# Optimization experiments

Measured on AMD Instinct MI355X. Metric: run time of the kernel, lower is better.

## Reference

```python
import jax, jax.numpy as jnp
import numpy as np

IN_DIMS = 4
DEPTH = 4
C = IN_DIMS + 1                     # channels after time augmentation
SIG = sum(C ** k for k in range(1, DEPTH + 1))  # 780
N, T = 64, 1024


def setup_inputs() -> dict:
    key = jax.random.key(0)
    k1, k2, k3, k4, k5 = jax.random.split(key, 5)
    batch = jax.random.normal(k1, (N, T, IN_DIMS), dtype=jnp.float32)
    s_c = 1.0 / np.sqrt(C)
    conv_w = jax.random.normal(k2, (C, C), dtype=jnp.float32) * s_c
    conv_b = jax.random.normal(k3, (C,), dtype=jnp.float32) * s_c
    s_l = 1.0 / np.sqrt(SIG)
    lin_w = jax.random.normal(k4, (SIG, SIG), dtype=jnp.float32) * s_l
    lin_b = jax.random.normal(k5, (SIG,), dtype=jnp.float32) * s_l
    return {"batch": batch, "conv_w": conv_w, "conv_b": conv_b,
            "lin_w": lin_w, "lin_b": lin_b}


def _stream_signature(path):
    """Streamed path signature with zero basepoint.

    path: (n, t, C). Returns (n, t, SIG) where entry t is the signature of
    the piecewise-linear path (0, path[0], ..., path[t]) truncated at DEPTH,
    levels flattened in lexicographic (row-major) order like signatory.
    """
    n = path.shape[0]
    # increments; basepoint=True means first increment is path[:,0] - 0
    dx = jnp.concatenate([path[:, :1, :], path[:, 1:, :] - path[:, :-1, :]], axis=1)
    init = tuple(jnp.zeros((n, C ** k), path.dtype) for k in range(1, DEPTH + 1))

    def step(levels, d):
        # exp(d) in the truncated tensor algebra: e_k = d^{(x)k} / k!
        e = [d]
        for k in range(2, DEPTH + 1):
            e.append((jnp.einsum('na,nb->nab', e[-1], d) / k).reshape(n, -1))
        # Chen: new_k = e_k + S_k + sum_{i=1}^{k-1} S_i (x) e_{k-i}
        new = []
        for k in range(1, DEPTH + 1):
            acc = levels[k - 1] + e[k - 1]
            for i in range(1, k):
                acc = acc + jnp.einsum('na,nb->nab', levels[i - 1], e[k - i - 1]).reshape(n, -1)
            new.append(acc)
        new = tuple(new)
        return new, jnp.concatenate(new, axis=-1)

    _, ys = jax.lax.scan(step, init, jnp.swapaxes(dx, 0, 1))  # ys: (t, n, SIG)
    return jnp.swapaxes(ys, 0, 1)


def reference(batch, conv_w, conv_b, lin_w, lin_b):
    n, t, _ = batch.shape
    # time augmentation: append channel arange(1,T+1)/T
    time = (jnp.arange(1, t + 1, dtype=batch.dtype) / t)[None, :, None]
    a = jnp.concatenate([batch, jnp.broadcast_to(time, (n, t, 1))], axis=-1)  # (n,t,C)
    # kernel-size-1 conv1d == pointwise linear over channels
    b = a @ conv_w.T + conv_b                                                  # (n,t,C)
    c = _stream_signature(b)                                                   # (n,t,SIG)
    # zero out the first stream entry (torch.concat of zeros with c[:,1:,:])
    c = jnp.concatenate([jnp.zeros((n, 1, SIG), c.dtype), c[:, 1:, :]], axis=1)
    return jnp.tanh(c @ lin_w.T + lin_b)
```

## Files before the change

kernel.cpp:

```cpp
#include <hip/hip_runtime.h>
#include <math.h>

#define N_B 64
#define T_LEN 1024
#define IN_D 4
#define CH 5
#define SIG 780
#define KP 800
#define SEG_LEN 16
#define N_SEG 64
#define SC_L1 1.0f
#define SC_L2 0.25f
#define SC_L3 0.0625f
#define SC_L4 0.015625f

typedef _Float16 f16x8 __attribute__((ext_vector_type(8)));
typedef float f32x4 __attribute__((ext_vector_type(4)));

typedef __attribute__((address_space(1))) const void* as1cp;
typedef __attribute__((address_space(3))) void* as3p;

__device__ __forceinline__ float fast_tanh(float x) {
  float ax = fabsf(x);
  float e = __expf(-2.0f * ax);
  float r = (1.0f - e) * __builtin_amdgcn_rcpf(1.0f + e);
  return copysignf(r, x);
}

__global__ __launch_bounds__(256) void conv_kernel(
    const float* __restrict__ batch,
    const float* __restrict__ conv_w,
    const float* __restrict__ conv_b,
    float* __restrict__ b_out) {
  int idx = blockIdx.x * blockDim.x + threadIdx.x;
  if (idx >= N_B * T_LEN) return;
  int t = idx & (T_LEN - 1);
  const float* a = batch + (size_t)idx * IN_D;
  float a0 = a[0], a1 = a[1], a2 = a[2], a3 = a[3];
  float tm = (float)(t + 1) / (float)T_LEN;
  float* o = b_out + (size_t)idx * CH;
#pragma unroll
  for (int j = 0; j < CH; ++j) {
    const float* w = conv_w + j * CH;
    float r = conv_b[j];
    r = fmaf(tm, w[4], r);
    r = fmaf(a3, w[3], r);
    r = fmaf(a2, w[2], r);
    r = fmaf(a1, w[1], r);
    r = fmaf(a0, w[0], r);
    o[j] = r;
  }
}

__global__ __launch_bounds__(320) void seg_kernel(
    const float* __restrict__ batch,
    const float* __restrict__ conv_w,
    const float* __restrict__ conv_b,
    float* __restrict__ P) {
  int s = blockIdx.x;
  int n = blockIdx.y;
  int tid = threadIdx.x;

  __shared__ float S[SIG];
  __shared__ float bc[(SEG_LEN + 1) * CH];
  __shared__ float dsh[SEG_LEN][CH];

  for (int i = tid; i < SIG; i += 320) S[i] = 0.0f;
  if (tid < (SEG_LEN + 1) * CH) {
    int r = s * SEG_LEN - 1 + tid / CH, ch = tid % CH;
    float v = 0.0f;
    if (r >= 0) {
      const float* a = batch + ((size_t)n * T_LEN + r) * IN_D;
      const float* w = conv_w + ch * CH;
      v = conv_b[ch];
      v = fmaf(a[0], w[0], v);
      v = fmaf(a[1], w[1], v);
      v = fmaf(a[2], w[2], v);
      v = fmaf(a[3], w[3], v);
      v = fmaf((float)(r + 1) * (1.0f / T_LEN), w[4], v);
    }
    bc[tid] = v;
  }
  __syncthreads();
  if (tid < SEG_LEN * CH) {
    int j = tid / CH, ch = tid % CH;
    dsh[j][ch] = bc[(j + 1) * CH + ch] - bc[j * CH + ch];
  }

  const int x0 = tid;
  const int x1 = tid + 320;
  const bool has1 = (tid < 305);
  const int a0i = x0 / 125, b0i = (x0 / 25) % 5, c0i = (x0 / 5) % 5, d0i = x0 % 5;
  const int a1i = x1 / 125, b1i = (x1 / 25) % 5, c1i = (x1 / 5) % 5, d1i = x1 % 5;
  const int s2_0 = x0 / 25, s3_0 = x0 / 5;
  const int s2_1 = x1 / 25, s3_1 = x1 / 5;
  const bool hasL3 = (tid < 125);
  const int ya = tid / 25, yb = (tid / 5) % 5, yc = tid % 5;
  const bool hasL2 = (tid < 25);
  const int za = tid / 5, zb = tid % 5;
  const bool hasL1 = (tid < CH);
  __syncthreads();

  for (int j = 0; j < SEG_LEN; ++j) {
    float n4_0, n4_1 = 0.0f, n3 = 0.0f, n2 = 0.0f, n1 = 0.0f;
    {
      float tH = fmaf(0.25f, dsh[j][a0i], S[a0i]);
      tH = fmaf((1.0f / 3.0f) * dsh[j][b0i], tH, S[5 + s2_0]);
      tH = fmaf(0.5f * dsh[j][c0i], tH, S[30 + s3_0]);
      n4_0 = fmaf(dsh[j][d0i], tH, S[155 + x0]);
    }
    if (has1) {
      float tH = fmaf(0.25f, dsh[j][a1i], S[a1i]);
      tH = fmaf((1.0f / 3.0f) * dsh[j][b1i], tH, S[5 + s2_1]);
      tH = fmaf(0.5f * dsh[j][c1i], tH, S[30 + s3_1]);
      n4_1 = fmaf(dsh[j][d1i], tH, S[155 + x1]);
    }
    if (hasL3) {
      float tH = fmaf((1.0f / 3.0f), dsh[j][ya], S[ya]);
      tH = fmaf(0.5f * dsh[j][yb], tH, S[5 + ya * 5 + yb]);
      n3 = fmaf(dsh[j][yc], tH, S[30 + tid]);
    }
    if (hasL2) {
      float tH = fmaf(0.5f, dsh[j][za], S[za]);
      n2 = fmaf(dsh[j][zb], tH, S[5 + tid]);
    }
    if (hasL1) n1 = S[tid] + dsh[j][tid];
    __syncthreads();
    S[155 + x0] = n4_0;
    if (has1) S[155 + x1] = n4_1;
    if (hasL3) S[30 + tid] = n3;
    if (hasL2) S[5 + tid] = n2;
    if (hasL1) S[tid] = n1;
    __syncthreads();
  }

  float* Pr = P + ((size_t)n * N_SEG + s) * SIG;
  for (int i = tid; i < SIG; i += 320) Pr[i] = S[i];
}

__global__ __launch_bounds__(640) void prefix_kernel(float* __restrict__ P) {
  int n = blockIdx.x;
  int tid = threadIdx.x;
  __shared__ float A[SIG];
  __shared__ float Bs[SIG];

  float* Pn = P + (size_t)n * N_SEG * SIG;
  for (int i = tid; i < SIG; i += 640) A[i] = Pn[i];
  int i0 = tid, i1 = tid + 640;
  float r0 = 0.f, r1 = 0.f;
  if (i0 < SIG) r0 = Pn[SIG + i0];
  if (i1 < SIG) r1 = Pn[SIG + i1];

  const int e4 = tid;
  const int q4a = e4 / 125, r125 = e4 % 125, r25 = e4 % 25, r5 = e4 % 5;
  const int e4d5 = e4 / 5, e4d25 = e4 / 25;
  const int e3 = tid;
  const int e3a = e3 / 25, e3r25 = e3 % 25, e3r5 = e3 % 5, e3d5 = e3 / 5;
  const int e2 = tid - 125;
  const int e1 = tid - 150;

  for (int s = 1; s < N_SEG; ++s) {
    if (i0 < SIG) Bs[i0] = r0;
    if (i1 < SIG) Bs[i1] = r1;
    __syncthreads();
    if (s + 1 < N_SEG) {
      const float* Pnx = Pn + (size_t)(s + 1) * SIG;
      if (i0 < SIG) r0 = Pnx[i0];
      if (i1 < SIG) r1 = Pnx[i1];
    }
    float v4 = 0.f, v3 = 0.f, v2 = 0.f, v1 = 0.f;
    if (tid < 625) {
      v4 = A[155 + e4] + Bs[155 + e4];
      v4 = fmaf(A[30 + e4d5], Bs[r5], v4);
      v4 = fmaf(A[5 + e4d25], Bs[5 + r25], v4);
      v4 = fmaf(A[q4a], Bs[30 + r125], v4);
    }
    if (tid < 125) {
      v3 = A[30 + e3] + Bs[30 + e3];
      v3 = fmaf(A[5 + e3d5], Bs[e3r5], v3);
      v3 = fmaf(A[e3a], Bs[5 + e3r25], v3);
    } else if (tid < 150) {
      v2 = A[5 + e2] + Bs[5 + e2];
      v2 = fmaf(A[e2 / 5], Bs[e2 % 5], v2);
    } else if (tid < 155) {
      v1 = A[e1] + Bs[e1];
    }
    __syncthreads();
    float* Po = Pn + (size_t)s * SIG;
    if (tid < 625) { A[155 + e4] = v4; Po[155 + e4] = v4; }
    if (tid < 125) { A[30 + e3] = v3; Po[30 + e3] = v3; }
    else if (tid < 150) { A[5 + e2] = v2; Po[5 + e2] = v2; }
    else if (tid < 155) { A[e1] = v1; Po[e1] = v1; }
  }
}

__global__ __launch_bounds__(320) void emit_kernel(
    const float* __restrict__ batch,
    const float* __restrict__ conv_w,
    const float* __restrict__ conv_b,
    const float* __restrict__ P,
    _Float16* __restrict__ c1,
    _Float16* __restrict__ c2) {
  int s = blockIdx.x;
  int n = blockIdx.y;
  int tid = threadIdx.x;

  __shared__ float S[SIG];
  __shared__ float bc[(SEG_LEN + 1) * CH];
  __shared__ float dsh[SEG_LEN][CH];
  __shared__ __align__(16) _Float16 row1[KP];
  __shared__ __align__(16) _Float16 row2[KP];

  if (s == 0) {
    for (int i = tid; i < SIG; i += 320) S[i] = 0.0f;
  } else {
    const float* Pr = P + ((size_t)n * N_SEG + (s - 1)) * SIG;
    for (int i = tid; i < SIG; i += 320) S[i] = Pr[i];
  }
  if (tid < (SEG_LEN + 1) * CH) {
    int r = s * SEG_LEN - 1 + tid / CH, ch = tid % CH;
    float v = 0.0f;
    if (r >= 0) {
      const float* a = batch + ((size_t)n * T_LEN + r) * IN_D;
      const float* w = conv_w + ch * CH;
      v = conv_b[ch];
      v = fmaf(a[0], w[0], v);
      v = fmaf(a[1], w[1], v);
      v = fmaf(a[2], w[2], v);
      v = fmaf(a[3], w[3], v);
      v = fmaf((float)(r + 1) * (1.0f / T_LEN), w[4], v);
    }
    bc[tid] = v;
  }
  if (tid < KP - SIG) {
    row1[SIG + tid] = (_Float16)0.0f;
    row2[SIG + tid] = (_Float16)0.0f;
  }
  __syncthreads();
  if (tid < SEG_LEN * CH) {
    int j = tid / CH, ch = tid % CH;
    dsh[j][ch] = bc[(j + 1) * CH + ch] - bc[j * CH + ch];
  }

  const int x0 = tid;
  const int x1 = tid + 320;
  const bool has1 = (tid < 305);
  const int a0i = x0 / 125, b0i = (x0 / 25) % 5, c0i = (x0 / 5) % 5, d0i = x0 % 5;
  const int a1i = x1 / 125, b1i = (x1 / 25) % 5, c1i = (x1 / 5) % 5, d1i = x1 % 5;
  const int s2_0 = x0 / 25, s3_0 = x0 / 5;
  const int s2_1 = x1 / 25, s3_1 = x1 / 5;
  const bool hasL3 = (tid < 125);
  const int ya = tid / 25, yb = (tid / 5) % 5, yc = tid % 5;
  const bool hasL2 = (tid < 25);
  const int za = tid / 5, zb = tid % 5;
  const bool hasL1 = (tid < CH);
  __syncthreads();

  for (int j = 0; j < SEG_LEN; ++j) {
    int t = s * SEG_LEN + j;
    float n4_0, n4_1 = 0.0f, n3 = 0.0f, n2 = 0.0f, n1 = 0.0f;
    {
      float tH = fmaf(0.25f, dsh[j][a0i], S[a0i]);
      tH = fmaf((1.0f / 3.0f) * dsh[j][b0i], tH, S[5 + s2_0]);
      tH = fmaf(0.5f * dsh[j][c0i], tH, S[30 + s3_0]);
      n4_0 = fmaf(dsh[j][d0i], tH, S[155 + x0]);
    }
    if (has1) {
      float tH = fmaf(0.25f, dsh[j][a1i], S[a1i]);
      tH = fmaf((1.0f / 3.0f) * dsh[j][b1i], tH, S[5 + s2_1]);
      tH = fmaf(0.5f * dsh[j][c1i], tH, S[30 + s3_1]);
      n4_1 = fmaf(dsh[j][d1i], tH, S[155 + x1]);
    }
    if (hasL3) {
      float tH = fmaf((1.0f / 3.0f), dsh[j][ya], S[ya]);
      tH = fmaf(0.5f * dsh[j][yb], tH, S[5 + ya * 5 + yb]);
      n3 = fmaf(dsh[j][yc], tH, S[30 + tid]);
    }
    if (hasL2) {
      float tH = fmaf(0.5f, dsh[j][za], S[za]);
      n2 = fmaf(dsh[j][zb], tH, S[5 + tid]);
    }
    if (hasL1) n1 = S[tid] + dsh[j][tid];
    __syncthreads();

    S[155 + x0] = n4_0;
    if (has1) S[155 + x1] = n4_1;
    if (hasL3) S[30 + tid] = n3;
    if (hasL2) S[5 + tid] = n2;
    if (hasL1) S[tid] = n1;

    float z = (t == 0) ? 0.0f : 1.0f;
    {
      float v = n4_0 * SC_L4 * z;
      _Float16 h = (_Float16)v;
      row1[155 + x0] = h; row2[155 + x0] = (_Float16)(v - (float)h);
    }
    if (has1) {
      float v = n4_1 * SC_L4 * z;
      _Float16 h = (_Float16)v;
      row1[155 + x1] = h; row2[155 + x1] = (_Float16)(v - (float)h);
    }
    if (hasL3) {
      float v = n3 * SC_L3 * z;
      _Float16 h = (_Float16)v;
      row1[30 + tid] = h; row2[30 + tid] = (_Float16)(v - (float)h);
    }
    if (hasL2) {
      float v = n2 * SC_L2 * z;
      _Float16 h = (_Float16)v;
      row1[5 + tid] = h; row2[5 + tid] = (_Float16)(v - (float)h);
    }
    if (hasL1) {
      float v = n1 * SC_L1 * z;
      _Float16 h = (_Float16)v;
      row1[tid] = h; row2[tid] = (_Float16)(v - (float)h);
    }
    __syncthreads();

    size_t base = ((size_t)n * T_LEN + t) * KP;
    if (tid < 100) {
      *(float4*)(c1 + base + tid * 8) = *(const float4*)&row1[tid * 8];
    } else if (tid < 200) {
      int c = tid - 100;
      *(float4*)(c2 + base + c * 8) = *(const float4*)&row2[c * 8];
    }
  }
}

__global__ __launch_bounds__(256) void wconv_kernel(
    const float* __restrict__ W,
    _Float16* __restrict__ w1,
    _Float16* __restrict__ w2) {
  int idx = blockIdx.x * blockDim.x + threadIdx.x;
  if (idx >= 896 * KP) return;
  int nn = idx / KP, k = idx % KP;
  float v = 0.0f;
  if (nn < SIG && k < SIG) {
    float sc = (k < 5) ? 1.0f : (k < 30) ? 4.0f : (k < 155) ? 16.0f : 64.0f;
    v = W[(size_t)nn * SIG + k] * sc;
  }
  _Float16 h = (_Float16)v;
  w1[idx] = h;
  w2[idx] = (_Float16)(v - (float)h);
}

__global__ __launch_bounds__(256) void gemm_mfma(
    const _Float16* __restrict__ A1p, const _Float16* __restrict__ A2p,
    const _Float16* __restrict__ B1p, const _Float16* __restrict__ B2p,
    const float* __restrict__ bias, float* __restrict__ out) {
  __shared__ _Float16 Al[2][2][128 * 32];
  __shared__ _Float16 Bl[2][2][128 * 32];

  int tid = threadIdx.x;
  int lane = tid & 63, wid = tid >> 6;
  int wm = wid >> 1, wn = wid & 1;
  int m0 = blockIdx.y * 128;
  int n0 = blockIdx.x * 128;

  f32x4 acc[4][4];
#pragma unroll
  for (int i = 0; i < 4; ++i)
#pragma unroll
    for (int j = 0; j < 4; ++j) acc[i][j] = (f32x4){0.f, 0.f, 0.f, 0.f};

  int sr = lane >> 2, scn = lane & 3;
  int swst = (sr ^ (sr >> 2)) & 3;
  int qg = scn ^ swst;
  int fr = lane & 15, fq = lane >> 4;
  int swf = (fr ^ (fr >> 2)) & 3;
  int fchunk = fq ^ swf;

  auto stage = [&](int kb, int buf) {
    int k0 = kb * 32;
#pragma unroll
    for (int i = 0; i < 2; ++i) {
      int rloc = wid * 16 + i * 64 + sr;
      size_t gA = (size_t)(m0 + rloc) * KP + k0 + qg * 8;
      size_t gB = (size_t)(n0 + rloc) * KP + k0 + qg * 8;
      int lb = (wid * 16 + i * 64) * 32;
      __builtin_amdgcn_global_load_lds((as1cp)(A1p + gA), (as3p)(&Al[buf][0][lb]), 16, 0, 0);
      __builtin_amdgcn_global_load_lds((as1cp)(A2p + gA), (as3p)(&Al[buf][1][lb]), 16, 0, 0);
      __builtin_amdgcn_global_load_lds((as1cp)(B1p + gB), (as3p)(&Bl[buf][0][lb]), 16, 0, 0);
      __builtin_amdgcn_global_load_lds((as1cp)(B2p + gB), (as3p)(&Bl[buf][1][lb]), 16, 0, 0);
    }
  };

  stage(0, 0);
  for (int kb = 0; kb < 25; ++kb) {
    int cur = kb & 1;
    __syncthreads();
    f16x8 a1[4], a2[4], b1[4], b2[4];
#pragma unroll
    for (int tm = 0; tm < 4; ++tm) {
      int off = (wm * 64 + tm * 16 + fr) * 32 + fchunk * 8;
      a1[tm] = *(const f16x8*)&Al[cur][0][off];
      a2[tm] = *(const f16x8*)&Al[cur][1][off];
    }
#pragma unroll
    for (int tn = 0; tn < 4; ++tn) {
      int off = (wn * 64 + tn * 16 + fr) * 32 + fchunk * 8;
      b1[tn] = *(const f16x8*)&Bl[cur][0][off];
      b2[tn] = *(const f16x8*)&Bl[cur][1][off];
    }
    if (kb < 24) stage(kb + 1, cur ^ 1);
#pragma unroll
    for (int tm = 0; tm < 4; ++tm)
#pragma unroll
      for (int tn = 0; tn < 4; ++tn) {
        acc[tm][tn] = __builtin_amdgcn_mfma_f32_16x16x32_f16(a1[tm], b1[tn], acc[tm][tn], 0, 0, 0);
        acc[tm][tn] = __builtin_amdgcn_mfma_f32_16x16x32_f16(a1[tm], b2[tn], acc[tm][tn], 0, 0, 0);
        acc[tm][tn] = __builtin_amdgcn_mfma_f32_16x16x32_f16(a2[tm], b1[tn], acc[tm][tn], 0, 0, 0);
      }
  }
  __syncthreads();

  float* ep = (float*)((wid < 2) ? (void*)&Al[0][0][0] : (void*)&Bl[0][0][0]);
  ep += (wid & 1) * 4096;

  float bv[4];
#pragma unroll
  for (int tn = 0; tn < 4; ++tn) {
    int nn = n0 + wn * 64 + tn * 16 + fr;
    bv[tn] = (nn < SIG) ? bias[nn] : 0.0f;
  }
#pragma unroll
  for (int h = 0; h < 2; ++h) {
#pragma unroll
    for (int tm2 = 0; tm2 < 2; ++tm2) {
      int tm = h * 2 + tm2;
#pragma unroll
      for (int tn = 0; tn < 4; ++tn) {
#pragma unroll
        for (int r = 0; r < 4; ++r) {
          int lr = tm2 * 16 + fq * 4 + r;
          int lc = tn * 16 + fr;
          ep[lr * 66 + lc] = fast_tanh(acc[tm][tn][r] + bv[tn]);
        }
      }
    }
#pragma unroll
    for (int p = 0; p < 2; ++p) {
      int lr = lane & 31;
      int ck = (lane >> 5) * 2 + p;
      int gm = m0 + wm * 64 + h * 32 + lr;
      int gc0 = n0 + wn * 64 + ck * 16;
#pragma unroll
      for (int q = 0; q < 4; ++q) {
        int col = gc0 + q * 4;
        if (col + 3 < SIG) {
          *(float4*)(out + (size_t)gm * SIG + col) =
              *(const float4*)&ep[lr * 66 + ck * 16 + q * 4];
        } else if (col < SIG) {
#pragma unroll
          for (int e = 0; e < 4; ++e) {
            int c2 = col + e;
            if (c2 < SIG) out[(size_t)gm * SIG + c2] = ep[lr * 66 + ck * 16 + q * 4 + e];
          }
        }
      }
    }
  }
}

__global__ __launch_bounds__(320) void sig_kernel_fb(
    const float* __restrict__ b_in, float* __restrict__ c_out) {
  int n = blockIdx.x;
  int tid = threadIdx.x;
  __shared__ float S[SIG];
  __shared__ float bc[64 * CH];
  __shared__ float dsh[CH];
  __shared__ float pb[CH];
  for (int i = tid; i < SIG; i += 320) S[i] = 0.0f;
  if (tid < CH) pb[tid] = 0.0f;
  const float* bn = b_in + (size_t)n * T_LEN * CH;
  float* cn = c_out + (size_t)n * T_LEN * SIG;
// ... 125 lines not shown
    }
  }
}

extern "C" void kernel_launch(void* const* d_in, const int* in_sizes, int n_in,
                              void* d_out, int out_size, void* d_ws, size_t ws_size,
                              hipStream_t stream) {
  const float* batch = (const float*)d_in[0];
  const float* conv_w = (const float*)d_in[1];
  const float* conv_b = (const float*)d_in[2];
  const float* lin_w = (const float*)d_in[3];
  const float* lin_b = (const float*)d_in[4];
  float* out = (float*)d_out;

  const size_t plane_elems = (size_t)N_B * T_LEN * KP;
  const size_t wplane_elems = (size_t)896 * KP;
  const size_t P_elems = (size_t)N_B * N_SEG * SIG;
  const size_t bp_elems = (size_t)N_B * T_LEN * CH;
  const size_t need_big = 2 * plane_elems * sizeof(_Float16) +
                          2 * wplane_elems * sizeof(_Float16) +
                          P_elems * sizeof(float);

  if (ws_size >= need_big) {
    _Float16* c1 = (_Float16*)d_ws;
    _Float16* c2 = c1 + plane_elems;
    _Float16* w1 = c2 + plane_elems;
    _Float16* w2 = w1 + wplane_elems;
    float* P = (float*)(w2 + wplane_elems);

    wconv_kernel<<<dim3((896 * KP + 255) / 256), dim3(256), 0, stream>>>(
        lin_w, w1, w2);
    seg_kernel<<<dim3(N_SEG, N_B), dim3(320), 0, stream>>>(batch, conv_w, conv_b, P);
    prefix_kernel<<<dim3(N_B), dim3(640), 0, stream>>>(P);
    emit_kernel<<<dim3(N_SEG, N_B), dim3(320), 0, stream>>>(
        batch, conv_w, conv_b, P, c1, c2);
    gemm_mfma<<<dim3(7, 512), dim3(256), 0, stream>>>(c1, c2, w1, w2, lin_b, out);
  } else {
    float* b_path = (float*)d_ws;
    float* c_sig = (float*)d_ws + bp_elems;
    conv_kernel<<<dim3((N_B * T_LEN + 255) / 256), dim3(256), 0, stream>>>(
        batch, conv_w, conv_b, b_path);
    sig_kernel_fb<<<dim3(N_B), dim3(320), 0, stream>>>(b_path, c_sig);
    gemm_tanh_fb<<<dim3((N_B * T_LEN) / BM, (SIG + BN - 1) / BN), dim3(256), 0, stream>>>(
        c_sig, lin_w, lin_b, out);
  }
}
```

Baseline: 724.5 us.

## Use single-wave segment kernels with register-held level 4 and loop GEMM over N tiles

```diff
diff --git a/kernel.cpp b/kernel.cpp
--- a/kernel.cpp
+++ b/kernel.cpp
@@ -7,6 +7,7 @@
 #define CH 5
 #define SIG 780
 #define KP 800
+#define NPAD 896
 #define SEG_LEN 16
 #define N_SEG 64
 #define SC_L1 1.0f
@@ -25,6 +26,507 @@
   float e = __expf(-2.0f * ax);
   float r = (1.0f - e) * __builtin_amdgcn_rcpf(1.0f + e);
   return copysignf(r, x);
+}
+
+__device__ __forceinline__ float sel5(float d0, float d1, float d2, float d3,
+                                      float d4, int i) {
+  float r = d0;
+  r = (i == 1) ? d1 : r;
+  r = (i == 2) ? d2 : r;
+  r = (i == 3) ? d3 : r;
+  r = (i == 4) ? d4 : r;
+  return r;
+}
+
+
+__global__ __launch_bounds__(64) void seg_wave(
+    const float* __restrict__ batch,
+    const float* __restrict__ conv_w,
+    const float* __restrict__ conv_b,
+    float* __restrict__ P) {
+  int s = blockIdx.x;
+  int n = blockIdx.y;
+  int lane = threadIdx.x;
+
+  __shared__ float S123[160];
+  __shared__ float bc[85];
+  __shared__ float dsh[SEG_LEN][CH];
+
+  for (int i = lane; i < 160; i += 64) S123[i] = 0.0f;
+#pragma unroll
+  for (int p = 0; p < 2; ++p) {
+    int e = lane + p * 64;
+    if (e < (SEG_LEN + 1) * CH) {
+      int r = s * SEG_LEN - 1 + e / CH, ch = e % CH;
+      float v = 0.0f;
+      if (r >= 0) {
+        const float* a = batch + ((size_t)n * T_LEN + r) * IN_D;
+        const float* w = conv_w + ch * CH;
+        v = conv_b[ch];
+        v = fmaf(a[0], w[0], v);
+        v = fmaf(a[1], w[1], v);
+        v = fmaf(a[2], w[2], v);
+        v = fmaf(a[3], w[3], v);
+        v = fmaf((float)(r + 1) * (1.0f / T_LEN), w[4], v);
+      }
+      bc[e] = v;
+    }
+  }
+  __syncthreads();
+#pragma unroll
+  for (int p = 0; p < 2; ++p) {
+    int e = lane + p * 64;
+    if (e < SEG_LEN * CH) dsh[e / CH][e % CH] = bc[e + CH] - bc[e];
+  }
+  __syncthreads();
+
+  const int xb = lane * 10;
+  const int a_lo = xb / 125, a_hi = (xb + 9) / 125;
+  const int s2_lo = xb / 25, s2_hi = (xb + 9) / 25;
+  const int s3_lo = 2 * lane, s3_hi = 2 * lane + 1;
+  const int b_lo = s2_lo % 5, b_hi = s2_hi % 5;
+  const int c_lo = s3_lo % 5, c_hi = s3_hi % 5;
+  const int q_a = a_lo * 125 + 125 - xb;
+  const int q_b = s2_lo * 25 + 25 - xb;
+  const int y0 = lane, y1 = lane + 64;
+  const bool hy0 = (y0 < 125), hy1 = (y1 < 125);
+  const int y0a = y0 / 25, y0s = y0 / 5, y0b = y0s % 5, y0c = y0 % 5;
+  const int y1a = y1 / 25, y1s = y1 / 5, y1b = y1s % 5, y1c = y1 % 5;
+  const bool hz = (lane < 25);
+  const int za = lane / 5, zb = lane % 5;
+  const bool h1 = (lane < 5);
+
+  float S4r[10];
+#pragma unroll
+  for (int q = 0; q < 10; ++q) S4r[q] = 0.0f;
+
+  for (int j = 0; j < SEG_LEN; ++j) {
+    float dr0 = dsh[j][0], dr1 = dsh[j][1], dr2 = dsh[j][2], dr3 = dsh[j][3],
+          dr4 = dsh[j][4];
+    float drA[5] = {dr0, dr1, dr2, dr3, dr4};
+    float da_l = sel5(dr0, dr1, dr2, dr3, dr4, a_lo);
+    float da_h = sel5(dr0, dr1, dr2, dr3, dr4, a_hi);
+    float db_l = sel5(dr0, dr1, dr2, dr3, dr4, b_lo);
+    float db_h = sel5(dr0, dr1, dr2, dr3, dr4, b_hi);
+    float dc_l = sel5(dr0, dr1, dr2, dr3, dr4, c_lo);
+    float dc_h = sel5(dr0, dr1, dr2, dr3, dr4, c_hi);
+    float s1_l = S123[a_lo], s1_h = S123[a_hi];
+    float s2v_l = S123[5 + s2_lo], s2v_h = S123[5 + s2_hi];
+    float s3v_l = S123[30 + s3_lo], s3v_h = S123[30 + s3_hi];
+
+#pragma unroll
+    for (int q = 0; q < 10; ++q) {
+      bool ua = (q >= q_a), ub = (q >= q_b);
+      float s1 = ua ? s1_h : s1_l, da = ua ? da_h : da_l;
+      float s2v = ub ? s2v_h : s2v_l, db = ub ? db_h : db_l;
+      float s3v = (q < 5) ? s3v_l : s3v_h;
+      float dc = (q < 5) ? dc_l : dc_h;
+      float dd = drA[q % 5];
+      float tH = fmaf(0.25f, da, s1);
+      tH = fmaf((1.0f / 3.0f) * db, tH, s2v);
+      tH = fmaf(0.5f * dc, tH, s3v);
+      S4r[q] = fmaf(dd, tH, S4r[q]);
+    }
+
+    float n3_0 = 0.f, n3_1 = 0.f, n2 = 0.f, n1 = 0.f;
+    if (hy0) {
+      float tH = fmaf((1.0f / 3.0f), drA[0] * 0.f + dsh[j][y0a], S123[y0a]);
+      tH = fmaf(0.5f * dsh[j][y0b], tH, S123[5 + y0s]);
+      n3_0 = fmaf(dsh[j][y0c], tH, S123[30 + y0]);
+    }
+    if (hy1) {
+      float tH = fmaf((1.0f / 3.0f), dsh[j][y1a], S123[y1a]);
+      tH = fmaf(0.5f * dsh[j][y1b], tH, S123[5 + y1s]);
+      n3_1 = fmaf(dsh[j][y1c], tH, S123[30 + y1]);
+    }
+    if (hz) {
+      float tH = fmaf(0.5f, dsh[j][za], S123[za]);
+      n2 = fmaf(dsh[j][zb], tH, S123[5 + lane]);
+    }
+    if (h1) n1 = S123[lane] + dsh[j][lane];
+    __syncthreads();
+    if (hy0) S123[30 + y0] = n3_0;
+    if (hy1) S123[30 + y1] = n3_1;
+    if (hz) S123[5 + lane] = n2;
+    if (h1) S123[lane] = n1;
+    __syncthreads();
+  }
+
+  float* Pr = P + ((size_t)n * N_SEG + s) * SIG;
+  for (int i = lane; i < 155; i += 64) Pr[i] = S123[i];
+#pragma unroll
+  for (int q = 0; q < 10; ++q) {
+    int x = xb + q;
+    if (x < 625) Pr[155 + x] = S4r[q];
+  }
+}
+
+__global__ __launch_bounds__(640) void prefix_kernel(float* __restrict__ P) {
+  int n = blockIdx.x;
+  int tid = threadIdx.x;
+  __shared__ float A[SIG];
+  __shared__ float Bs[SIG];
+
+  float* Pn = P + (size_t)n * N_SEG * SIG;
+  for (int i = tid; i < SIG; i += 640) A[i] = Pn[i];
+  int i0 = tid, i1 = tid + 640;
+  float r0 = 0.f, r1 = 0.f;
+  if (i0 < SIG) r0 = Pn[SIG + i0];
+  if (i1 < SIG) r1 = Pn[SIG + i1];
+
+  const int e4 = tid;
+  const int q4a = e4 / 125, r125 = e4 % 125, r25 = e4 % 25, r5 = e4 % 5;
+  const int e4d5 = e4 / 5, e4d25 = e4 / 25;
+  const int e3 = tid;
+  const int e3a = e3 / 25, e3r25 = e3 % 25, e3r5 = e3 % 5, e3d5 = e3 / 5;
+  const int e2 = tid - 125;
+  const int e1 = tid - 150;
+
+  for (int s = 1; s < N_SEG; ++s) {
+    if (i0 < SIG) Bs[i0] = r0;
+    if (i1 < SIG) Bs[i1] = r1;
+    __syncthreads();
+    if (s + 1 < N_SEG) {
+      const float* Pnx = Pn + (size_t)(s + 1) * SIG;
+      if (i0 < SIG) r0 = Pnx[i0];
+      if (i1 < SIG) r1 = Pnx[i1];
+    }
+    float v4 = 0.f, v3 = 0.f, v2 = 0.f, v1 = 0.f;
+    if (tid < 625) {
+      v4 = A[155 + e4] + Bs[155 + e4];
+      v4 = fmaf(A[30 + e4d5], Bs[r5], v4);
+      v4 = fmaf(A[5 + e4d25], Bs[5 + r25], v4);
+      v4 = fmaf(A[q4a], Bs[30 + r125], v4);
+    }
+    if (tid < 125) {
+      v3 = A[30 + e3] + Bs[30 + e3];
+      v3 = fmaf(A[5 + e3d5], Bs[e3r5], v3);
+      v3 = fmaf(A[e3a], Bs[5 + e3r25], v3);
+    } else if (tid < 150) {
+      v2 = A[5 + e2] + Bs[5 + e2];
+      v2 = fmaf(A[e2 / 5], Bs[e2 % 5], v2);
+    } else if (tid < 155) {
+      v1 = A[e1] + Bs[e1];
+    }
+    __syncthreads();
+    float* Po = Pn + (size_t)s * SIG;
+    if (tid < 625) { A[155 + e4] = v4; Po[155 + e4] = v4; }
+    if (tid < 125) { A[30 + e3] = v3; Po[30 + e3] = v3; }
+    else if (tid < 150) { A[5 + e2] = v2; Po[5 + e2] = v2; }
+    else if (tid < 155) { A[e1] = v1; Po[e1] = v1; }
+  }
+}
+
+__global__ __launch_bounds__(64) void emit_wave(
+    const float* __restrict__ batch,
+    const float* __restrict__ conv_w,
+    const float* __restrict__ conv_b,
+    const float* __restrict__ P,
+    _Float16* __restrict__ c1,
+    _Float16* __restrict__ c2) {
+  int s = blockIdx.x;
+  int n = blockIdx.y;
+  int lane = threadIdx.x;
+
+  __shared__ float S123[160];
+  __shared__ float bc[85];
+  __shared__ float dsh[SEG_LEN][CH];
+  __shared__ __align__(16) _Float16 row1[KP];
+  __shared__ __align__(16) _Float16 row2[KP];
+
+  const int xb = lane * 10;
+  float S4r[10];
+  if (s == 0) {
+    for (int i = lane; i < 160; i += 64) S123[i] = 0.0f;
+#pragma unroll
+    for (int q = 0; q < 10; ++q) S4r[q] = 0.0f;
+  } else {
+    const float* Pr = P + ((size_t)n * N_SEG + (s - 1)) * SIG;
+    for (int i = lane; i < 155; i += 64) S123[i] = Pr[i];
+    if (lane < 5) S123[155 + lane] = 0.0f;
+#pragma unroll
+    for (int q = 0; q < 10; ++q) {
+      int x = xb + q;
+      S4r[q] = (x < 625) ? Pr[155 + x] : 0.0f;
+    }
+  }
+#pragma unroll
+  for (int p = 0; p < 2; ++p) {
+    int e = lane + p * 64;
+    if (e < (SEG_LEN + 1) * CH) {
+      int r = s * SEG_LEN - 1 + e / CH, ch = e % CH;
+      float v = 0.0f;
+      if (r >= 0) {
+        const float* a = batch + ((size_t)n * T_LEN + r) * IN_D;
+        const float* w = conv_w + ch * CH;
+        v = conv_b[ch];
+        v = fmaf(a[0], w[0], v);
+        v = fmaf(a[1], w[1], v);
+        v = fmaf(a[2], w[2], v);
+        v = fmaf(a[3], w[3], v);
+        v = fmaf((float)(r + 1) * (1.0f / T_LEN), w[4], v);
+      }
+      bc[e] = v;
+    }
+  }
+  if (lane < KP - SIG) {
+    row1[SIG + lane] = (_Float16)0.0f;
+    row2[SIG + lane] = (_Float16)0.0f;
+  }
+  __syncthreads();
+#pragma unroll
+  for (int p = 0; p < 2; ++p) {
+    int e = lane + p * 64;
+    if (e < SEG_LEN * CH) dsh[e / CH][e % CH] = bc[e + CH] - bc[e];
+  }
+  __syncthreads();
+
+  const int a_lo = xb / 125, a_hi = (xb + 9) / 125;
+  const int s2_lo = xb / 25, s2_hi = (xb + 9) / 25;
+  const int s3_lo = 2 * lane, s3_hi = 2 * lane + 1;
+  const int b_lo = s2_lo % 5, b_hi = s2_hi % 5;
+  const int c_lo = s3_lo % 5, c_hi = s3_hi % 5;
+  const int q_a = a_lo * 125 + 125 - xb;
+  const int q_b = s2_lo * 25 + 25 - xb;
+  const int y0 = lane, y1 = lane + 64;
+  const bool hy0 = (y0 < 125), hy1 = (y1 < 125);
+  const int y0a = y0 / 25, y0s = y0 / 5, y0b = y0s % 5, y0c = y0 % 5;
+  const int y1a = y1 / 25, y1s = y1 / 5, y1b = y1s % 5, y1c = y1 % 5;
+  const bool hz = (lane < 25);
+  const int za = lane / 5, zb = lane % 5;
+  const bool h1 = (lane < 5);
+
+  for (int j = 0; j < SEG_LEN; ++j) {
+    int t = s * SEG_LEN + j;
+    float zf = (t == 0) ? 0.0f : 1.0f;
+    float dr0 = dsh[j][0], dr1 = dsh[j][1], dr2 = dsh[j][2], dr3 = dsh[j][3],
+          dr4 = dsh[j][4];
+    float drA[5] = {dr0, dr1, dr2, dr3, dr4};
+    float da_l = sel5(dr0, dr1, dr2, dr3, dr4, a_lo);
+    float da_h = sel5(dr0, dr1, dr2, dr3, dr4, a_hi);
+    float db_l = sel5(dr0, dr1, dr2, dr3, dr4, b_lo);
+    float db_h = sel5(dr0, dr1, dr2, dr3, dr4, b_hi);
+    float dc_l = sel5(dr0, dr1, dr2, dr3, dr4, c_lo);
+    float dc_h = sel5(dr0, dr1, dr2, dr3, dr4, c_hi);
+    float s1_l = S123[a_lo], s1_h = S123[a_hi];
+    float s2v_l = S123[5 + s2_lo], s2v_h = S123[5 + s2_hi];
+    float s3v_l = S123[30 + s3_lo], s3v_h = S123[30 + s3_hi];
+
+#pragma unroll
+    for (int q = 0; q < 10; ++q) {
+      bool ua = (q >= q_a), ub = (q >= q_b);
+      float s1 = ua ? s1_h : s1_l, da = ua ? da_h : da_l;
+      float s2v = ub ? s2v_h : s2v_l, db = ub ? db_h : db_l;
+      float s3v = (q < 5) ? s3v_l : s3v_h;
+      float dc = (q < 5) ? dc_l : dc_h;
+      float dd = drA[q % 5];
+      float tH = fmaf(0.25f, da, s1);
+      tH = fmaf((1.0f / 3.0f) * db, tH, s2v);
+      tH = fmaf(0.5f * dc, tH, s3v);
+      S4r[q] = fmaf(dd, tH, S4r[q]);
+    }
+
+    float n3_0 = 0.f, n3_1 = 0.f, n2 = 0.f, n1 = 0.f;
+    if (hy0) {
+      float tH = fmaf((1.0f / 3.0f), dsh[j][y0a], S123[y0a]);
+      tH = fmaf(0.5f * dsh[j][y0b], tH, S123[5 + y0s]);
+      n3_0 = fmaf(dsh[j][y0c], tH, S123[30 + y0]);
+    }
+    if (hy1) {
+      float tH = fmaf((1.0f / 3.0f), dsh[j][y1a], S123[y1a]);
+      tH = fmaf(0.5f * dsh[j][y1b], tH, S123[5 + y1s]);
+      n3_1 = fmaf(dsh[j][y1c], tH, S123[30 + y1]);
+    }
+    if (hz) {
+      float tH = fmaf(0.5f, dsh[j][za], S123[za]);
+      n2 = fmaf(dsh[j][zb], tH, S123[5 + lane]);
+    }
+    if (h1) n1 = S123[lane] + dsh[j][lane];
+    __syncthreads();
+
+    if (hy0) S123[30 + y0] = n3_0;
+    if (hy1) S123[30 + y1] = n3_1;
+    if (hz) S123[5 + lane] = n2;
+    if (h1) S123[lane] = n1;
+#pragma unroll
+    for (int q = 0; q < 10; ++q) {
+      int x = xb + q;
+      if (x < 625) {
+        float v = S4r[q] * (SC_L4 * zf);
+        _Float16 h = (_Float16)v;
+        row1[155 + x] = h;
+        row2[155 + x] = (_Float16)(v - (float)h);
+      }
+    }
+    if (hy0) {
+      float v = n3_0 * (SC_L3 * zf);
+      _Float16 h = (_Float16)v;
+      row1[30 + y0] = h; row2[30 + y0] = (_Float16)(v - (float)h);
+    }
+    if (hy1) {
+      float v = n3_1 * (SC_L3 * zf);
+      _Float16 h = (_Float16)v;
+      row1[30 + y1] = h; row2[30 + y1] = (_Float16)(v - (float)h);
+    }
+    if (hz) {
+      float v = n2 * (SC_L2 * zf);
+      _Float16 h = (_Float16)v;
+      row1[5 + lane] = h; row2[5 + lane] = (_Float16)(v - (float)h);
+    }
+    if (h1) {
+      float v = n1 * (SC_L1 * zf);
+      _Float16 h = (_Float16)v;
+      row1[lane] = h; row2[lane] = (_Float16)(v - (float)h);
+    }
+    __syncthreads();
+
+    size_t base = ((size_t)n * T_LEN + t) * KP;
+    *(float4*)(c1 + base + lane * 8) = *(const float4*)&row1[lane * 8];
+    *(float4*)(c2 + base + lane * 8) = *(const float4*)&row2[lane * 8];
+    if (lane < 36) {
+      *(float4*)(c1 + base + (64 + lane) * 8) = *(const float4*)&row1[(64 + lane) * 8];
+      *(float4*)(c2 + base + (64 + lane) * 8) = *(const float4*)&row2[(64 + lane) * 8];
+    }
+  }
+}
+
+__global__ __launch_bounds__(256) void wconv_kernel(
+    const float* __restrict__ W,
+    _Float16* __restrict__ w1,
+    _Float16* __restrict__ w2) {
+  int idx = blockIdx.x * blockDim.x + threadIdx.x;
+  if (idx >= NPAD * KP) return;
+  int nn = idx / KP, k = idx % KP;
+  float v = 0.0f;
+  if (nn < SIG && k < SIG) {
+    float sc = (k < 5) ? 1.0f : (k < 30) ? 4.0f : (k < 155) ? 16.0f : 64.0f;
+    v = W[(size_t)nn * SIG + k] * sc;
+  }
+  _Float16 h = (_Float16)v;
+  w1[idx] = h;
+  w2[idx] = (_Float16)(v - (float)h);
+}
+
+__global__ __launch_bounds__(256) void gemm_mfma(
+    const _Float16* __restrict__ A1p, const _Float16* __restrict__ A2p,
+    const _Float16* __restrict__ B1p, const _Float16* __restrict__ B2p,
+    const float* __restrict__ bias, float* __restrict__ out) {
+  __shared__ _Float16 Al[2][2][128 * 32];
+  __shared__ _Float16 Bl[2][2][128 * 32];
+
+  int tid = threadIdx.x;
+  int lane = tid & 63, wid = tid >> 6;
+  int wm = wid >> 1, wn = wid & 1;
+  int m0 = blockIdx.x * 128;
+
+  int sr = lane >> 2, scn = lane & 3;
+  int swst = (sr ^ (sr >> 2)) & 3;
+  int qg = scn ^ swst;
+  int fr = lane & 15, fq = lane >> 4;
+  int swf = (fr ^ (fr >> 2)) & 3;
+  int fchunk = fq ^ swf;
+
+  auto stage = [&](int n0, int kb, int buf) {
+    int k0 = kb * 32;
+#pragma unroll
+    for (int i = 0; i < 2; ++i) {
+      int rloc = wid * 16 + i * 64 + sr;
+      size_t gA = (size_t)(m0 + rloc) * KP + k0 + qg * 8;
+      size_t gB = (size_t)(n0 + rloc) * KP + k0 + qg * 8;
+      int lb = (wid * 16 + i * 64) * 32;
+      __builtin_amdgcn_global_load_lds((as1cp)(A1p + gA), (as3p)(&Al[buf][0][lb]), 16, 0, 0);
+      __builtin_amdgcn_global_load_lds((as1cp)(A2p + gA), (as3p)(&Al[buf][1][lb]), 16, 0, 0);
+      __builtin_amdgcn_global_load_lds((as1cp)(B1p + gB), (as3p)(&Bl[buf][0][lb]), 16, 0, 0);
+      __builtin_amdgcn_global_load_lds((as1cp)(B2p + gB), (as3p)(&Bl[buf][1][lb]), 16, 0, 0);
+    }
+  };
+
+  for (int nt = 0; nt < 7; ++nt) {
+    int n0 = nt * 128;
+
+    f32x4 acc[4][4];
+#pragma unroll
+    for (int i = 0; i < 4; ++i)
+#pragma unroll
+      for (int j = 0; j < 4; ++j) acc[i][j] = (f32x4){0.f, 0.f, 0.f, 0.f};
+
+    stage(n0, 0, 0);
+    for (int kb = 0; kb < 25; ++kb) {
+      int cur = kb & 1;
+      __syncthreads();
+      f16x8 a1[4], a2[4], b1[4], b2[4];
+#pragma unroll
+      for (int tm = 0; tm < 4; ++tm) {
+        int off = (wm * 64 + tm * 16 + fr) * 32 + fchunk * 8;
+        a1[tm] = *(const f16x8*)&Al[cur][0][off];
+        a2[tm] = *(const f16x8*)&Al[cur][1][off];
+      }
+#pragma unroll
+      for (int tn = 0; tn < 4; ++tn) {
+        int off = (wn * 64 + tn * 16 + fr) * 32 + fchunk * 8;
+        b1[tn] = *(const f16x8*)&Bl[cur][0][off];
+        b2[tn] = *(const f16x8*)&Bl[cur][1][off];
+      }
+      if (kb < 24) stage(n0, kb + 1, cur ^ 1);
+#pragma unroll
+      for (int tm = 0; tm < 4; ++tm)
+#pragma unroll
+        for (int tn = 0; tn < 4; ++tn) {
+          acc[tm][tn] = __builtin_amdgcn_mfma_f32_16x16x32_f16(a1[tm], b1[tn], acc[tm][tn], 0, 0, 0);
+          acc[tm][tn] = __builtin_amdgcn_mfma_f32_16x16x32_f16(a1[tm], b2[tn], acc[tm][tn], 0, 0, 0);
+          acc[tm][tn] = __builtin_amdgcn_mfma_f32_16x16x32_f16(a2[tm], b1[tn], acc[tm][tn], 0, 0, 0);
+        }
+    }
+    __syncthreads();
+
+    float* ep = (float*)((wid < 2) ? (void*)&Al[0][0][0] : (void*)&Bl[0][0][0]);
+    ep += (wid & 1) * 4096;
+
+    float bv[4];
+#pragma unroll
+    for (int tn = 0; tn < 4; ++tn) {
+      int nn = n0 + wn * 64 + tn * 16 + fr;
+      bv[tn] = (nn < SIG) ? bias[nn] : 0.0f;
+    }
+#pragma unroll
+    for (int h = 0; h < 2; ++h) {
+#pragma unroll
+      for (int tm2 = 0; tm2 < 2; ++tm2) {
+        int tm = h * 2 + tm2;
+#pragma unroll
+        for (int tn = 0; tn < 4; ++tn) {
+#pragma unroll
+          for (int r = 0; r < 4; ++r) {
+            int lr = tm2 * 16 + fq * 4 + r;
+            int lc = tn * 16 + fr;
+            ep[lr * 66 + lc] = fast_tanh(acc[tm][tn][r] + bv[tn]);
+          }
+        }
+      }
+#pragma unroll
+      for (int p = 0; p < 2; ++p) {
+        int lr = lane & 31;
+        int ck = (lane >> 5) * 2 + p;
+        int gm = m0 + wm * 64 + h * 32 + lr;
+        int gc0 = n0 + wn * 64 + ck * 16;
+#pragma unroll
+        for (int q = 0; q < 4; ++q) {
+          int col = gc0 + q * 4;
+          if (col + 3 < SIG) {
+            *(float4*)(out + (size_t)gm * SIG + col) =
+                *(const float4*)&ep[lr * 66 + ck * 16 + q * 4];
+          } else if (col < SIG) {
+#pragma unroll
+            for (int e = 0; e < 4; ++e) {
+              int c2 = col + e;
+              if (c2 < SIG) out[(size_t)gm * SIG + c2] = ep[lr * 66 + ck * 16 + q * 4 + e];
+            }
+          }
+        }
+      }
+    }
+    __syncthreads();
+  }
 }
 
 __global__ __launch_bounds__(256) void conv_kernel(
@@ -49,416 +551,6 @@
     r = fmaf(a1, w[1], r);
     r = fmaf(a0, w[0], r);
     o[j] = r;
-  }
-}
-
-__global__ __launch_bounds__(320) void seg_kernel(
-    const float* __restrict__ batch,
-    const float* __restrict__ conv_w,
-    const float* __restrict__ conv_b,
-    float* __restrict__ P) {
-  int s = blockIdx.x;
-  int n = blockIdx.y;
-  int tid = threadIdx.x;
-
-  __shared__ float S[SIG];
-  __shared__ float bc[(SEG_LEN + 1) * CH];
-  __shared__ float dsh[SEG_LEN][CH];
-
-  for (int i = tid; i < SIG; i += 320) S[i] = 0.0f;
-  if (tid < (SEG_LEN + 1) * CH) {
-    int r = s * SEG_LEN - 1 + tid / CH, ch = tid % CH;
-    float v = 0.0f;
-    if (r >= 0) {
-      const float* a = batch + ((size_t)n * T_LEN + r) * IN_D;
-      const float* w = conv_w + ch * CH;
-      v = conv_b[ch];
-      v = fmaf(a[0], w[0], v);
-      v = fmaf(a[1], w[1], v);
-      v = fmaf(a[2], w[2], v);
-      v = fmaf(a[3], w[3], v);
-      v = fmaf((float)(r + 1) * (1.0f / T_LEN), w[4], v);
-    }
-    bc[tid] = v;
-  }
-  __syncthreads();
-  if (tid < SEG_LEN * CH) {
-    int j = tid / CH, ch = tid % CH;
-    dsh[j][ch] = bc[(j + 1) * CH + ch] - bc[j * CH + ch];
-  }
-
-  const int x0 = tid;
-  const int x1 = tid + 320;
-  const bool has1 = (tid < 305);
-  const int a0i = x0 / 125, b0i = (x0 / 25) % 5, c0i = (x0 / 5) % 5, d0i = x0 % 5;
-  const int a1i = x1 / 125, b1i = (x1 / 25) % 5, c1i = (x1 / 5) % 5, d1i = x1 % 5;
-  const int s2_0 = x0 / 25, s3_0 = x0 / 5;
-  const int s2_1 = x1 / 25, s3_1 = x1 / 5;
-  const bool hasL3 = (tid < 125);
-  const int ya = tid / 25, yb = (tid / 5) % 5, yc = tid % 5;
-  const bool hasL2 = (tid < 25);
-  const int za = tid / 5, zb = tid % 5;
-  const bool hasL1 = (tid < CH);
-  __syncthreads();
-
-  for (int j = 0; j < SEG_LEN; ++j) {
-    float n4_0, n4_1 = 0.0f, n3 = 0.0f, n2 = 0.0f, n1 = 0.0f;
-    {
-      float tH = fmaf(0.25f, dsh[j][a0i], S[a0i]);
-      tH = fmaf((1.0f / 3.0f) * dsh[j][b0i], tH, S[5 + s2_0]);
-      tH = fmaf(0.5f * dsh[j][c0i], tH, S[30 + s3_0]);
-      n4_0 = fmaf(dsh[j][d0i], tH, S[155 + x0]);
-    }
-    if (has1) {
-      float tH = fmaf(0.25f, dsh[j][a1i], S[a1i]);
-      tH = fmaf((1.0f / 3.0f) * dsh[j][b1i], tH, S[5 + s2_1]);
-      tH = fmaf(0.5f * dsh[j][c1i], tH, S[30 + s3_1]);
-      n4_1 = fmaf(dsh[j][d1i], tH, S[155 + x1]);
-    }
-    if (hasL3) {
-      float tH = fmaf((1.0f / 3.0f), dsh[j][ya], S[ya]);
-      tH = fmaf(0.5f * dsh[j][yb], tH, S[5 + ya * 5 + yb]);
-      n3 = fmaf(dsh[j][yc], tH, S[30 + tid]);
-    }
-    if (hasL2) {
-      float tH = fmaf(0.5f, dsh[j][za], S[za]);
-      n2 = fmaf(dsh[j][zb], tH, S[5 + tid]);
-    }
-    if (hasL1) n1 = S[tid] + dsh[j][tid];
-    __syncthreads();
-    S[155 + x0] = n4_0;
-    if (has1) S[155 + x1] = n4_1;
-    if (hasL3) S[30 + tid] = n3;
-    if (hasL2) S[5 + tid] = n2;
-    if (hasL1) S[tid] = n1;
-    __syncthreads();
-  }
-
-  float* Pr = P + ((size_t)n * N_SEG + s) * SIG;
-  for (int i = tid; i < SIG; i += 320) Pr[i] = S[i];
-}
-
-__global__ __launch_bounds__(640) void prefix_kernel(float* __restrict__ P) {
-  int n = blockIdx.x;
-  int tid = threadIdx.x;
-  __shared__ float A[SIG];
-  __shared__ float Bs[SIG];
-
-  float* Pn = P + (size_t)n * N_SEG * SIG;
-  for (int i = tid; i < SIG; i += 640) A[i] = Pn[i];
-  int i0 = tid, i1 = tid + 640;
-  float r0 = 0.f, r1 = 0.f;
-  if (i0 < SIG) r0 = Pn[SIG + i0];
-  if (i1 < SIG) r1 = Pn[SIG + i1];
-
-  const int e4 = tid;
-  const int q4a = e4 / 125, r125 = e4 % 125, r25 = e4 % 25, r5 = e4 % 5;
-  const int e4d5 = e4 / 5, e4d25 = e4 / 25;
-  const int e3 = tid;
-  const int e3a = e3 / 25, e3r25 = e3 % 25, e3r5 = e3 % 5, e3d5 = e3 / 5;
-  const int e2 = tid - 125;
-  const int e1 = tid - 150;
-
-  for (int s = 1; s < N_SEG; ++s) {
-    if (i0 < SIG) Bs[i0] = r0;
-    if (i1 < SIG) Bs[i1] = r1;
-    __syncthreads();
-    if (s + 1 < N_SEG) {
-      const float* Pnx = Pn + (size_t)(s + 1) * SIG;
-      if (i0 < SIG) r0 = Pnx[i0];
-      if (i1 < SIG) r1 = Pnx[i1];
-    }
-    float v4 = 0.f, v3 = 0.f, v2 = 0.f, v1 = 0.f;
-    if (tid < 625) {
-      v4 = A[155 + e4] + Bs[155 + e4];
-      v4 = fmaf(A[30 + e4d5], Bs[r5], v4);
-      v4 = fmaf(A[5 + e4d25], Bs[5 + r25], v4);
-      v4 = fmaf(A[q4a], Bs[30 + r125], v4);
-    }
-    if (tid < 125) {
-      v3 = A[30 + e3] + Bs[30 + e3];
-      v3 = fmaf(A[5 + e3d5], Bs[e3r5], v3);
-      v3 = fmaf(A[e3a], Bs[5 + e3r25], v3);
-    } else if (tid < 150) {
-      v2 = A[5 + e2] + Bs[5 + e2];
-      v2 = fmaf(A[e2 / 5], Bs[e2 % 5], v2);
-    } else if (tid < 155) {
-      v1 = A[e1] + Bs[e1];
-    }
-    __syncthreads();
-    float* Po = Pn + (size_t)s * SIG;
-    if (tid < 625) { A[155 + e4] = v4; Po[155 + e4] = v4; }
-    if (tid < 125) { A[30 + e3] = v3; Po[30 + e3] = v3; }
-    else if (tid < 150) { A[5 + e2] = v2; Po[5 + e2] = v2; }
-    else if (tid < 155) { A[e1] = v1; Po[e1] = v1; }
-  }
-}
-
-__global__ __launch_bounds__(320) void emit_kernel(
-    const float* __restrict__ batch,
-    const float* __restrict__ conv_w,
-    const float* __restrict__ conv_b,
-    const float* __restrict__ P,
-    _Float16* __restrict__ c1,
-    _Float16* __restrict__ c2) {
-  int s = blockIdx.x;
-  int n = blockIdx.y;
-  int tid = threadIdx.x;
-
-  __shared__ float S[SIG];
-  __shared__ float bc[(SEG_LEN + 1) * CH];
-  __shared__ float dsh[SEG_LEN][CH];
-  __shared__ __align__(16) _Float16 row1[KP];
-  __shared__ __align__(16) _Float16 row2[KP];
-
-  if (s == 0) {
-    for (int i = tid; i < SIG; i += 320) S[i] = 0.0f;
-  } else {
-    const float* Pr = P + ((size_t)n * N_SEG + (s - 1)) * SIG;
-    for (int i = tid; i < SIG; i += 320) S[i] = Pr[i];
-  }
-  if (tid < (SEG_LEN + 1) * CH) {
-    int r = s * SEG_LEN - 1 + tid / CH, ch = tid % CH;
-    float v = 0.0f;
-    if (r >= 0) {
-      const float* a = batch + ((size_t)n * T_LEN + r) * IN_D;
-      const float* w = conv_w + ch * CH;
-      v = conv_b[ch];
-      v = fmaf(a[0], w[0], v);
-      v = fmaf(a[1], w[1], v);
-      v = fmaf(a[2], w[2], v);
-      v = fmaf(a[3], w[3], v);
-      v = fmaf((float)(r + 1) * (1.0f / T_LEN), w[4], v);
-    }
-    bc[tid] = v;
-  }
-  if (tid < KP - SIG) {
-    row1[SIG + tid] = (_Float16)0.0f;
-    row2[SIG + tid] = (_Float16)0.0f;
-  }
-  __syncthreads();
-  if (tid < SEG_LEN * CH) {
-    int j = tid / CH, ch = tid % CH;
-    dsh[j][ch] = bc[(j + 1) * CH + ch] - bc[j * CH + ch];
-  }
-
-  const int x0 = tid;
-  const int x1 = tid + 320;
-  const bool has1 = (tid < 305);
-  const int a0i = x0 / 125, b0i = (x0 / 25) % 5, c0i = (x0 / 5) % 5, d0i = x0 % 5;
-  const int a1i = x1 / 125, b1i = (x1 / 25) % 5, c1i = (x1 / 5) % 5, d1i = x1 % 5;
-  const int s2_0 = x0 / 25, s3_0 = x0 / 5;
-  const int s2_1 = x1 / 25, s3_1 = x1 / 5;
-  const bool hasL3 = (tid < 125);
-  const int ya = tid / 25, yb = (tid / 5) % 5, yc = tid % 5;
-  const bool hasL2 = (tid < 25);
-  const int za = tid / 5, zb = tid % 5;
-  const bool hasL1 = (tid < CH);
-  __syncthreads();
-
-  for (int j = 0; j < SEG_LEN; ++j) {
-    int t = s * SEG_LEN + j;
-    float n4_0, n4_1 = 0.0f, n3 = 0.0f, n2 = 0.0f, n1 = 0.0f;
-    {
-      float tH = fmaf(0.25f, dsh[j][a0i], S[a0i]);
-      tH = fmaf((1.0f / 3.0f) * dsh[j][b0i], tH, S[5 + s2_0]);
-      tH = fmaf(0.5f * dsh[j][c0i], tH, S[30 + s3_0]);
-      n4_0 = fmaf(dsh[j][d0i], tH, S[155 + x0]);
-    }
-    if (has1) {
-      float tH = fmaf(0.25f, dsh[j][a1i], S[a1i]);
-      tH = fmaf((1.0f / 3.0f) * dsh[j][b1i], tH, S[5 + s2_1]);
-      tH = fmaf(0.5f * dsh[j][c1i], tH, S[30 + s3_1]);
-      n4_1 = fmaf(dsh[j][d1i], tH, S[155 + x1]);
-    }
-    if (hasL3) {
-      float tH = fmaf((1.0f / 3.0f), dsh[j][ya], S[ya]);
-      tH = fmaf(0.5f * dsh[j][yb], tH, S[5 + ya * 5 + yb]);
-      n3 = fmaf(dsh[j][yc], tH, S[30 + tid]);
-    }
-    if (hasL2) {
-      float tH = fmaf(0.5f, dsh[j][za], S[za]);
-      n2 = fmaf(dsh[j][zb], tH, S[5 + tid]);
-    }
-    if (hasL1) n1 = S[tid] + dsh[j][tid];
-    __syncthreads();
-
-    S[155 + x0] = n4_0;
-    if (has1) S[155 + x1] = n4_1;
-    if (hasL3) S[30 + tid] = n3;
-    if (hasL2) S[5 + tid] = n2;
-    if (hasL1) S[tid] = n1;
-
-    float z = (t == 0) ? 0.0f : 1.0f;
-    {
-      float v = n4_0 * SC_L4 * z;
-      _Float16 h = (_Float16)v;
-      row1[155 + x0] = h; row2[155 + x0] = (_Float16)(v - (float)h);
-    }
-    if (has1) {
-      float v = n4_1 * SC_L4 * z;
-      _Float16 h = (_Float16)v;
-      row1[155 + x1] = h; row2[155 + x1] = (_Float16)(v - (float)h);
-    }
-    if (hasL3) {
-      float v = n3 * SC_L3 * z;
-      _Float16 h = (_Float16)v;
-      row1[30 + tid] = h; row2[30 + tid] = (_Float16)(v - (float)h);
-    }
-    if (hasL2) {
-      float v = n2 * SC_L2 * z;
-      _Float16 h = (_Float16)v;
-      row1[5 + tid] = h; row2[5 + tid] = (_Float16)(v - (float)h);
-    }
-    if (hasL1) {
-      float v = n1 * SC_L1 * z;
-      _Float16 h = (_Float16)v;
-      row1[tid] = h; row2[tid] = (_Float16)(v - (float)h);
-    }
-    __syncthreads();
-
-    size_t base = ((size_t)n * T_LEN + t) * KP;
-    if (tid < 100) {
-      *(float4*)(c1 + base + tid * 8) = *(const float4*)&row1[tid * 8];
-    } else if (tid < 200) {
-      int c = tid - 100;
-      *(float4*)(c2 + base + c * 8) = *(const float4*)&row2[c * 8];
-    }
-  }
-}
-
-__global__ __launch_bounds__(256) void wconv_kernel(
-    const float* __restrict__ W,
-    _Float16* __restrict__ w1,
-    _Float16* __restrict__ w2) {
-  int idx = blockIdx.x * blockDim.x + threadIdx.x;
-  if (idx >= 896 * KP) return;
-  int nn = idx / KP, k = idx % KP;
-  float v = 0.0f;
-  if (nn < SIG && k < SIG) {
-    float sc = (k < 5) ? 1.0f : (k < 30) ? 4.0f : (k < 155) ? 16.0f : 64.0f;
-    v = W[(size_t)nn * SIG + k] * sc;
-  }
-  _Float16 h = (_Float16)v;
-  w1[idx] = h;
-  w2[idx] = (_Float16)(v - (float)h);
-}
-
-__global__ __launch_bounds__(256) void gemm_mfma(
-    const _Float16* __restrict__ A1p, const _Float16* __restrict__ A2p,
-    const _Float16* __restrict__ B1p, const _Float16* __restrict__ B2p,
-    const float* __restrict__ bias, float* __restrict__ out) {
-  __shared__ _Float16 Al[2][2][128 * 32];
-  __shared__ _Float16 Bl[2][2][128 * 32];
-
-  int tid = threadIdx.x;
-  int lane = tid & 63, wid = tid >> 6;
-  int wm = wid >> 1, wn = wid & 1;
-  int m0 = blockIdx.y * 128;
-  int n0 = blockIdx.x * 128;
-
-  f32x4 acc[4][4];
-#pragma unroll
-  for (int i = 0; i < 4; ++i)
-#pragma unroll
-    for (int j = 0; j < 4; ++j) acc[i][j] = (f32x4){0.f, 0.f, 0.f, 0.f};
-
-  int sr = lane >> 2, scn = lane & 3;
-  int swst = (sr ^ (sr >> 2)) & 3;
-  int qg = scn ^ swst;
-  int fr = lane & 15, fq = lane >> 4;
-  int swf = (fr ^ (fr >> 2)) & 3;
-  int fchunk = fq ^ swf;
-
-  auto stage = [&](int kb, int buf) {
-    int k0 = kb * 32;
-#pragma unroll
-    for (int i = 0; i < 2; ++i) {
-      int rloc = wid * 16 + i * 64 + sr;
-      size_t gA = (size_t)(m0 + rloc) * KP + k0 + qg * 8;
-      size_t gB = (size_t)(n0 + rloc) * KP + k0 + qg * 8;
-      int lb = (wid * 16 + i * 64) * 32;
-      __builtin_amdgcn_global_load_lds((as1cp)(A1p + gA), (as3p)(&Al[buf][0][lb]), 16, 0, 0);
-      __builtin_amdgcn_global_load_lds((as1cp)(A2p + gA), (as3p)(&Al[buf][1][lb]), 16, 0, 0);
-      __builtin_amdgcn_global_load_lds((as1cp)(B1p + gB), (as3p)(&Bl[buf][0][lb]), 16, 0, 0);
-      __builtin_amdgcn_global_load_lds((as1cp)(B2p + gB), (as3p)(&Bl[buf][1][lb]), 16, 0, 0);
-    }
-  };
-
-  stage(0, 0);
-  for (int kb = 0; kb < 25; ++kb) {
-    int cur = kb & 1;
-    __syncthreads();
-    f16x8 a1[4], a2[4], b1[4], b2[4];
-#pragma unroll
-    for (int tm = 0; tm < 4; ++tm) {
-      int off = (wm * 64 + tm * 16 + fr) * 32 + fchunk * 8;
-      a1[tm] = *(const f16x8*)&Al[cur][0][off];
-      a2[tm] = *(const f16x8*)&Al[cur][1][off];
-    }
-#pragma unroll
-    for (int tn = 0; tn < 4; ++tn) {
-      int off = (wn * 64 + tn * 16 + fr) * 32 + fchunk * 8;
-      b1[tn] = *(const f16x8*)&Bl[cur][0][off];
-      b2[tn] = *(const f16x8*)&Bl[cur][1][off];
-    }
-    if (kb < 24) stage(kb + 1, cur ^ 1);
-#pragma unroll
-    for (int tm = 0; tm < 4; ++tm)
-#pragma unroll
-      for (int tn = 0; tn < 4; ++tn) {
-        acc[tm][tn] = __builtin_amdgcn_mfma_f32_16x16x32_f16(a1[tm], b1[tn], acc[tm][tn], 0, 0, 0);
-        acc[tm][tn] = __builtin_amdgcn_mfma_f32_16x16x32_f16(a1[tm], b2[tn], acc[tm][tn], 0, 0, 0);
-        acc[tm][tn] = __builtin_amdgcn_mfma_f32_16x16x32_f16(a2[tm], b1[tn], acc[tm][tn], 0, 0, 0);
-      }
-  }
-  __syncthreads();
-
-  float* ep = (float*)((wid < 2) ? (void*)&Al[0][0][0] : (void*)&Bl[0][0][0]);
-  ep += (wid & 1) * 4096;
-
-  float bv[4];
-#pragma unroll
-  for (int tn = 0; tn < 4; ++tn) {
-    int nn = n0 + wn * 64 + tn * 16 + fr;
-    bv[tn] = (nn < SIG) ? bias[nn] : 0.0f;
-  }
-#pragma unroll
-  for (int h = 0; h < 2; ++h) {
-#pragma unroll
-    for (int tm2 = 0; tm2 < 2; ++tm2) {
-      int tm = h * 2 + tm2;
-#pragma unroll
-      for (int tn = 0; tn < 4; ++tn) {
-#pragma unroll
-        for (int r = 0; r < 4; ++r) {
-          int lr = tm2 * 16 + fq * 4 + r;
-          int lc = tn * 16 + fr;
-          ep[lr * 66 + lc] = fast_tanh(acc[tm][tn][r] + bv[tn]);
-        }
-      }
-    }
-#pragma unroll
-    for (int p = 0; p < 2; ++p) {
-      int lr = lane & 31;
-      int ck = (lane >> 5) * 2 + p;
-      int gm = m0 + wm * 64 + h * 32 + lr;
-      int gc0 = n0 + wn * 64 + ck * 16;
-#pragma unroll
-      for (int q = 0; q < 4; ++q) {
-        int col = gc0 + q * 4;
-        if (col + 3 < SIG) {
-          *(float4*)(out + (size_t)gm * SIG + col) =
-              *(const float4*)&ep[lr * 66 + ck * 16 + q * 4];
-        } else if (col < SIG) {
-#pragma unroll
-          for (int e = 0; e < 4; ++e) {
-            int c2 = col + e;
-            if (c2 < SIG) out[(size_t)gm * SIG + c2] = ep[lr * 66 + ck * 16 + q * 4 + e];
-          }
-        }
-      }
-    }
   }
 }
 
@@ -614,7 +706,7 @@
   float* out = (float*)d_out;
 
   const size_t plane_elems = (size_t)N_B * T_LEN * KP;
-  const size_t wplane_elems = (size_t)896 * KP;
+  const size_t wplane_elems = (size_t)NPAD * KP;
   const size_t P_elems = (size_t)N_B * N_SEG * SIG;
   const size_t bp_elems = (size_t)N_B * T_LEN * CH;
   const size_t need_big = 2 * plane_elems * sizeof(_Float16) +
@@ -628,13 +720,13 @@
     _Float16* w2 = w1 + wplane_elems;
     float* P = (float*)(w2 + wplane_elems);
 
-    wconv_kernel<<<dim3((896 * KP + 255) / 256), dim3(256), 0, stream>>>(
+    wconv_kernel<<<dim3((NPAD * KP + 255) / 256), dim3(256), 0, stream>>>(
         lin_w, w1, w2);
-    seg_kernel<<<dim3(N_SEG, N_B), dim3(320), 0, stream>>>(batch, conv_w, conv_b, P);
+    seg_wave<<<dim3(N_SEG, N_B), dim3(64), 0, stream>>>(batch, conv_w, conv_b, P);
     prefix_kernel<<<dim3(N_B), dim3(640), 0, stream>>>(P);
-    emit_kernel<<<dim3(N_SEG, N_B), dim3(320), 0, stream>>>(
+    emit_wave<<<dim3(N_SEG, N_B), dim3(64), 0, stream>>>(
         batch, conv_w, conv_b, P, c1, c2);
-    gemm_mfma<<<dim3(7, 512), dim3(256), 0, stream>>>(c1, c2, w1, w2, lin_b, out);
+    gemm_mfma<<<dim3(512), dim3(256), 0, stream>>>(c1, c2, w1, w2, lin_b, out);
   } else {
     float* b_path = (float*)d_ws;
     float* c_sig = (float*)d_ws + bp_elems;
```

Result: no change. 733.1 us (+1.2%).
